# Optimization experiments

Measured on AMD Instinct MI355X. Metric: run time of the kernel, lower is better.

Reference implementation:

```python
import math
import jax, jax.numpy as jnp
import numpy as np
from jax.scipy.linalg import solve_triangular

K, D, Q = 512, 2048, 8
B = 8192
EPS = 1e-5
RHO0 = math.log(math.exp(1.0) - 1.0)  # softplus^-1(1.0), matches psi_init=scale_init=1.0


def setup_inputs() -> dict:
    key = jax.random.key(0)
    k1, k2, k3, k4, k5 = jax.random.split(key, 5)
    x = jax.random.normal(k1, (B, D), dtype=jnp.float32)
    mu = jax.random.normal(k2, (K, D), dtype=jnp.float32)          # centroids
    dir_raw = jax.random.normal(k3, (K, D, Q), dtype=jnp.float32) / math.sqrt(D)
    scale_rho = jnp.full((K, Q), RHO0, dtype=jnp.float32) + 0.01 * jax.random.normal(k4, (K, Q), dtype=jnp.float32)
    psi_rho = jnp.full((D,), RHO0, dtype=jnp.float32) + 0.01 * jax.random.normal(k5, (D,), dtype=jnp.float32)
    pi_logits = jnp.zeros((K,), dtype=jnp.float32)
    return {"x": x, "mu": mu, "dir_raw": dir_raw, "scale_rho": scale_rho,
            "psi_rho": psi_rho, "pi_logits": pi_logits}


def _nll(x, mu, dir_raw, scale_rho, psi_rho, pi_logits):
    Dd = x.shape[1]
    q = dir_raw.shape[2]
    # diagonal noise (shared across components since psi_per_component=False)
    psi = jax.nn.softplus(psi_rho) + EPS                      # (D,)
    psi_inv = 1.0 / psi                                       # (D,)
    # factor loadings W_k = normalize(dir_raw, dim=1) * softplus(scale)
    n = jnp.maximum(jnp.linalg.norm(dir_raw, axis=1, keepdims=True), EPS)
    W = (dir_raw / n) * jax.nn.softplus(scale_rho)[:, None, :]  # (K, D, q)
    # Woodbury inner matrix M_k = I + W^T Psi^{-1} W and its Cholesky
    A = W * jnp.sqrt(psi_inv)[None, :, None]                  # (K, D, q)
    M = jnp.einsum('kdi,kdj->kij', A, A) + jnp.eye(q, dtype=W.dtype)[None]
    L = jnp.linalg.cholesky(M)                                # (K, q, q) lower
    # quadratic form pieces
    xT_Pinv_x = (x ** 2) @ psi_inv                            # (B,)
    xT_Pinv_mu = x @ (psi_inv[None, :] * mu).T                # (B, K)
    muT_Pinv_mu = jnp.sum(mu ** 2 * psi_inv[None, :], axis=-1)  # (K,)
    quad_Psi = xT_Pinv_x[:, None] - 2.0 * xT_Pinv_mu + muT_Pinv_mu[None, :]
    PinvW = psi_inv[None, :, None] * W                        # (K, D, q)
    WT_Pinv_x = jnp.einsum('bd,kdq->bkq', x, PinvW)           # (B, K, q)
    WT_Pinv_mu = jnp.einsum('kd,kdq->kq', mu, PinvW)          # (K, q)
    v = WT_Pinv_x - WT_Pinv_mu[None, :, :]                    # (B, K, q)
    # Ez = M^{-1} v via the Cholesky factor (batched over K, rhs over B)
    vT = jnp.transpose(v, (1, 2, 0))                          # (K, q, B)
    y = solve_triangular(L, vT, lower=True)
    EzT = solve_triangular(jnp.swapaxes(L, -1, -2), y, lower=False)
    Ez = jnp.transpose(EzT, (2, 0, 1))                        # (B, K, q)
    quad = quad_Psi - jnp.sum(v * Ez, axis=-1)                # (B, K)
    # log-determinants via Woodbury: log|C| = log|Psi| + log|M|
    logdet_Psi = jnp.sum(jnp.log(psi))                        # scalar (shared psi)
    logdet_M = 2.0 * jnp.sum(jnp.log(jnp.diagonal(L, axis1=-2, axis2=-1)), axis=-1)  # (K,)
    logdet_C = logdet_Psi + logdet_M                          # (K,)
    ll = -0.5 * (Dd * math.log(2.0 * math.pi) + logdet_C[None, :] + quad)  # (B, K)
    log_pi = jax.nn.log_softmax(pi_logits)
    logp = jax.scipy.special.logsumexp(ll + log_pi[None, :], axis=1)  # (B,)
    return jnp.mean(-logp)


def reference(x, mu, dir_raw, scale_rho, psi_rho, pi_logits):
    return _nll(x, mu, dir_raw, scale_rho, psi_rho, pi_logits)
```

## Files before the change

kernel.cpp:

```cpp
#include <hip/hip_runtime.h>

constexpr int Bn = 8192;
constexpr int Dd = 2048;
constexpr int Kk = 512;
constexpr int Qq = 8;
constexpr int Nn = Kk * 9;
constexpr float DLOG2PI = 3763.9722f;

constexpr int BM = 256, BN = 144, BK = 128;

constexpr float SX = 16.f;
constexpr float SW = 64.f;
constexpr float SG = 16.f;
constexpr float INV_UW = 1.f / (16.f * 64.f);
constexpr float INV_UG = 1.f / (16.f * 16.f);

constexpr size_t OFF_PSI   = 0;
constexpr size_t OFF_LDP   = 8192;
constexpr size_t OFF_LOGPI = 8448;
constexpr size_t OFF_OFFK  = 10752;
constexpr size_t OFF_MINV  = 13056;
constexpr size_t OFF_XPX   = 144384;
constexpr size_t OFF_XBF   = 177408;
constexpr size_t OFF_GT    = 33731840;
constexpr size_t OFF_LL    = 52606208;
constexpr size_t OFF_PART  = 69383424;

typedef float f32x4 __attribute__((ext_vector_type(4)));
typedef int   i32x4v __attribute__((ext_vector_type(4)));
typedef int   i32x8v __attribute__((ext_vector_type(8)));

__device__ inline float softplusf(float x) {
  return fmaxf(x, 0.f) + log1pf(expf(-fabsf(x)));
}
__device__ inline unsigned short f2bf(float x) {
  unsigned int u = __builtin_bit_cast(unsigned int, x);
  u = (u + 0x7fffu + ((u >> 16) & 1u)) >> 16;
  return (unsigned short)u;
}
__device__ inline float bf2f(unsigned short u) {
  unsigned int v = ((unsigned int)u) << 16;
  return __builtin_bit_cast(float, v);
}
__device__ inline unsigned char f2fp8(float x) {
  int v = __builtin_amdgcn_cvt_pk_fp8_f32(x, 0.f, 0, false);
  return (unsigned char)(v & 0xff);
}
__device__ inline void glds16(const unsigned char* g, char* l) {
  __builtin_amdgcn_global_load_lds(
      (const __attribute__((address_space(1))) unsigned int*)g,
      (__attribute__((address_space(3))) unsigned int*)l, 16, 0, 0);
}
__device__ inline i32x8v ld_frag(const char* rowp, int quad, int s8) {
  i32x4v lo = *(const i32x4v*)(rowp + (((2 * quad)     ^ s8) * 16));
  i32x4v hi = *(const i32x4v*)(rowp + (((2 * quad + 1) ^ s8) * 16));
  i32x8v r;
  r[0] = lo[0]; r[1] = lo[1]; r[2] = lo[2]; r[3] = lo[3];
  r[4] = hi[0]; r[5] = hi[1]; r[6] = hi[2]; r[7] = hi[3];
  return r;
}

__global__ __launch_bounds__(256) void prep_psi(
    const float* __restrict__ psi_rho, const float* __restrict__ pi_logits,
    float* __restrict__ psi_inv, float* __restrict__ logdetPsi,
    float* __restrict__ logpi) {
  __shared__ float red[256];
  int t = threadIdx.x;
  float acc = 0.f;
  for (int d = t; d < Dd; d += 256) {
    float p = softplusf(psi_rho[d]) + 1e-5f;
    psi_inv[d] = 1.f / p;
    acc += logf(p);
  }
  red[t] = acc;
  __syncthreads();
  for (int s = 128; s > 0; s >>= 1) { if (t < s) red[t] += red[t + s]; __syncthreads(); }
  if (t == 0) *logdetPsi = red[0];
  __syncthreads();
  float mx = -3.4e38f;
  for (int i = t; i < Kk; i += 256) mx = fmaxf(mx, pi_logits[i]);
  red[t] = mx;
  __syncthreads();
  for (int s = 128; s > 0; s >>= 1) { if (t < s) red[t] = fmaxf(red[t], red[t + s]); __syncthreads(); }
  mx = red[0];
  __syncthreads();
  float se = 0.f;
  for (int i = t; i < Kk; i += 256) se += expf(pi_logits[i] - mx);
  red[t] = se;
  __syncthreads();
  for (int s = 128; s > 0; s >>= 1) { if (t < s) red[t] += red[t + s]; __syncthreads(); }
  float lse = mx + logf(red[0]);
  for (int i = t; i < Kk; i += 256) logpi[i] = pi_logits[i] - lse;
}

__global__ __launch_bounds__(256) void prep_k(
    const float* __restrict__ mu, const float* __restrict__ dir_raw,
    const float* __restrict__ scale_rho, const float* __restrict__ psi_inv,
    const float* __restrict__ logdetPsi, const float* __restrict__ logpi,
    float* __restrict__ offk, float* __restrict__ Minv,
    unsigned char* __restrict__ Gq) {
  __shared__ unsigned short sDir[Dd * 8];
  __shared__ float sPwmd[Dd];
  int k = blockIdx.x, t = threadIdx.x, lane = t & 63, w = t >> 6;
  float vals[53];
#pragma unroll
  for (int i = 0; i < 53; i++) vals[i] = 0.f;
  const float4* dirp = (const float4*)(dir_raw + (size_t)k * Dd * Qq);
  for (int d = t; d < Dd; d += 256) {
    float4 da = dirp[d * 2], db = dirp[d * 2 + 1];
    float dir8[8] = {da.x, da.y, da.z, da.w, db.x, db.y, db.z, db.w};
    float pw = psi_inv[d];
    float md = mu[(size_t)k * Dd + d];
    int c = 0;
#pragma unroll
    for (int i = 0; i < 8; i++) {
      float dip = dir8[i] * pw;
#pragma unroll
      for (int j = 0; j < 8; j++) {
        if (j < i) continue;
        vals[c] += dip * dir8[j]; c++;
      }
    }
#pragma unroll
    for (int q = 0; q < 8; q++) vals[36 + q] += dir8[q] * dir8[q];
    float mp = md * pw;
#pragma unroll
    for (int q = 0; q < 8; q++) vals[44 + q] += mp * dir8[q];
    vals[52] += md * mp;
#pragma unroll
    for (int q = 0; q < 8; q++) sDir[d * 8 + q] = f2bf(pw * dir8[q]);
    sPwmd[d] = mp;
  }
  __shared__ float redk[4 * 53];
#pragma unroll
  for (int v = 0; v < 53; v++) {
    float val = vals[v];
#pragma unroll
    for (int o = 32; o; o >>= 1) val += __shfl_down(val, o, 64);
    if (lane == 0) redk[w * 53 + v] = val;
  }
  __syncthreads();
  __shared__ float R[53];
  __shared__ float sAl[8], sAh[8];
  if (t < 53) R[t] = redk[t] + redk[53 + t] + redk[106 + t] + redk[159 + t];
  __syncthreads();
  if (t == 0) {
    float Sf[8][8];
    {
      int c2 = 0;
#pragma unroll
      for (int i = 0; i < 8; i++) {
#pragma unroll
        for (int j = 0; j < 8; j++) {
          if (j < i) continue;
          float v = R[c2++]; Sf[i][j] = v; Sf[j][i] = v;
        }
      }
    }
    float alpha[8];
#pragma unroll
    for (int q = 0; q < 8; q++) {
      float nr = fmaxf(sqrtf(R[36 + q]), 1e-5f);
      alpha[q] = softplusf(scale_rho[(size_t)k * 8 + q]) / nr;
    }
    float Mm[8][8];
#pragma unroll
    for (int i = 0; i < 8; i++)
#pragma unroll
      for (int j = 0; j < 8; j++)
        Mm[i][j] = alpha[i] * alpha[j] * Sf[i][j] + (i == j ? 1.f : 0.f);
    float L[8][8], Ld[8];
#pragma unroll
    for (int i = 0; i < 8; i++) {
#pragma unroll
      for (int j = 0; j < 8; j++) {
        if (j > i) continue;
        float s2 = Mm[i][j];
#pragma unroll
        for (int p = 0; p < 8; p++) { if (p < j) s2 -= L[i][p] * L[j][p]; }
        if (i == j) { L[i][i] = sqrtf(s2); Ld[i] = 1.f / L[i][i]; }
        else        L[i][j] = s2 * Ld[j];
      }
    }
    float logdetM = 0.f;
#pragma unroll
    for (int i = 0; i < 8; i++) logdetM += 2.f * logf(L[i][i]);
    float wv[8];
#pragma unroll
    for (int q = 0; q < 8; q++) wv[q] = alpha[q] * R[44 + q];
    float y[8], h[8];
#pragma unroll
    for (int i = 0; i < 8; i++) {
      float s2 = wv[i];
#pragma unroll
      for (int p = 0; p < 8; p++) { if (p < i) s2 -= L[i][p] * y[p]; }
      y[i] = s2 * Ld[i];
    }
#pragma unroll
    for (int i = 7; i >= 0; i--) {
      float s2 = y[i];
#pragma unroll
      for (int p = 0; p < 8; p++) { if (p > i) s2 -= L[p][i] * h[p]; }
      h[i] = s2 * Ld[i];
    }
    float cc = R[52];
#pragma unroll
    for (int q = 0; q < 8; q++) cc -= wv[q] * h[q];
#pragma unroll
    for (int col = 0; col < 8; col++) {
      float yy[8], z[8];
#pragma unroll
      for (int i = 0; i < 8; i++) {
        float s2 = (i == col) ? 1.f : 0.f;
#pragma unroll
        for (int p = 0; p < 8; p++) { if (p < i) s2 -= L[i][p] * yy[p]; }
        yy[i] = s2 * Ld[i];
      }
#pragma unroll
      for (int i = 7; i >= 0; i--) {
        float s2 = yy[i];
#pragma unroll
        for (int p = 0; p < 8; p++) { if (p > i) s2 -= L[p][i] * z[p]; }
        z[i] = s2 * Ld[i];
      }
#pragma unroll
      for (int r2 = 0; r2 < 8; r2++) Minv[(size_t)k * 64 + r2 * 8 + col] = z[r2];
    }
    offk[k] = -0.5f * (DLOG2PI + logdetPsi[0] + logdetM + cc) + logpi[k];
#pragma unroll
    for (int q = 0; q < 8; q++) { sAl[q] = alpha[q]; sAh[q] = alpha[q] * h[q]; }
  }
  __syncthreads();
  float al[8], ah[8];
#pragma unroll
  for (int q = 0; q < 8; q++) { al[q] = sAl[q]; ah[q] = sAh[q]; }
  for (int d = t; d < Dd; d += 256) {
    float pd[8];
#pragma unroll
    for (int q = 0; q < 8; q++) pd[q] = bf2f(sDir[d * 8 + q]);
    float gs = 0.f;
#pragma unroll
    for (int q = 0; q < 8; q++) {
      Gq[((size_t)(k * 9 + q)) * Dd + d] = f2fp8(SW * al[q] * pd[q]);
      gs += ah[q] * pd[q];
    }
    Gq[((size_t)(k * 9 + 8)) * Dd + d] = f2fp8(SG * (sPwmd[d] - gs));
  }
}

__global__ __launch_bounds__(256) void prep_x(
    const float* __restrict__ x, const float* __restrict__ psi_inv,
    unsigned char* __restrict__ xq, float* __restrict__ xPx) {
  int b = blockIdx.x, t = threadIdx.x, lane = t & 63, w = t >> 6;
  const float4* xr = (const float4*)(x + (size_t)b * Dd);
  const float4* pr = (const float4*)psi_inv;
  float4 v0 = xr[2 * t], v1 = xr[2 * t + 1];
  float4 p0 = pr[2 * t], p1 = pr[2 * t + 1];
  float acc = v0.x * v0.x * p0.x + v0.y * v0.y * p0.y + v0.z * v0.z * p0.z + v0.w * v0.w * p0.w
            + v1.x * v1.x * p1.x + v1.y * v1.y * p1.y + v1.z * v1.z * p1.z + v1.w * v1.w * p1.w;
  unsigned int q0 = (unsigned int)__builtin_amdgcn_cvt_pk_fp8_f32(SX * v0.x, SX * v0.y, 0, false);
  q0 = (unsigned int)__builtin_amdgcn_cvt_pk_fp8_f32(SX * v0.z, SX * v0.w, (int)q0, true);
  unsigned int q1 = (unsigned int)__builtin_amdgcn_cvt_pk_fp8_f32(SX * v1.x, SX * v1.y, 0, false);
  q1 = (unsigned int)__builtin_amdgcn_cvt_pk_fp8_f32(SX * v1.z, SX * v1.w, (int)q1, true);
  uint2 o; o.x = q0; o.y = q1;
  *(uint2*)(xq + (size_t)b * Dd + t * 8) = o;
#pragma unroll
  for (int s2 = 32; s2; s2 >>= 1) acc += __shfl_down(acc, s2, 64);
  __shared__ float r4[4];
  if (lane == 0) r4[w] = acc;
  __syncthreads();
  if (t == 0) xPx[b] = r4[0] + r4[1] + r4[2] + r4[3];
}

__global__ __launch_bounds__(256, 2) void gemm_ll(
    const unsigned char* __restrict__ xq, const unsigned char* __restrict__ Gq,
    const float* __restrict__ Minv, const float* __restrict__ offk,
    const float* __restrict__ xPx, float* __restrict__ ll) {
  __shared__ char smem[55424];
  float* Cs    = (float*)smem;
  float* sMinv = (float*)(smem + 51200);
  float* sOff  = (float*)(smem + 51200 + 4160);

  int t = threadIdx.x, lane = t & 63, w = t >> 6;
  int m0 = blockIdx.y * BM;
  int n0 = blockIdx.x * BN;
  int comp0 = blockIdx.x * 16;

  for (int i = t; i < 1024; i += 256) {
    int cl = i >> 6, idx = i & 63;
    sMinv[cl * 65 + idx] = Minv[(size_t)comp0 * 64 + i];
  }
  if (t < 16) sOff[t] = offk[comp0 + t];

  f32x4 acc[4][9];
  f32x4 zero = {0.f, 0.f, 0.f, 0.f};
#pragma unroll
  for (int mt = 0; mt < 4; mt++)
#pragma unroll
    for (int nt = 0; nt < 9; nt++) acc[mt][nt] = zero;

  int rr  = lane >> 3;
  int cph = lane & 7;
  int csw = cph ^ rr;
  int quad = lane >> 4, r16 = lane & 15;
  int s8 = r16 & 7;

#pragma unroll 1
  for (int k0 = 0; k0 < Dd; k0 += BK) {
    __syncthreads();
#pragma unroll
    for (int j = 0; j < 8; ++j) {
      int jj = w * 8 + j;
      glds16(xq + (size_t)(m0 + jj * 8 + rr) * Dd + k0 + csw * 16,
             smem + jj * 1024);
    }
    for (int jj = w; jj < 18; jj += 4) {
      glds16(Gq + (size_t)(n0 + jj * 8 + rr) * Dd + k0 + csw * 16,
             smem + 32768 + jj * 1024);
    }
    __syncthreads();
    i32x8v a0 = ld_frag(smem + (w * 64 +      r16) * 128, quad, s8);
    i32x8v a1 = ld_frag(smem + (w * 64 + 16 + r16) * 128, quad, s8);
    i32x8v a2 = ld_frag(smem + (w * 64 + 32 + r16) * 128, quad, s8);
    i32x8v a3 = ld_frag(smem + (w * 64 + 48 + r16) * 128, quad, s8);
#pragma unroll
    for (int nt = 0; nt < 9; ++nt) {
      i32x8v bv = ld_frag(smem + 32768 + (nt * 16 + r16) * 128, quad, s8);
      acc[0][nt] = __builtin_amdgcn_mfma_scale_f32_16x16x128_f8f6f4(
          a0, bv, acc[0][nt], 0, 0, 0, 0x7f7f7f7f, 0, 0x7f7f7f7f);
      acc[1][nt] = __builtin_amdgcn_mfma_scale_f32_16x16x128_f8f6f4(
          a1, bv, acc[1][nt], 0, 0, 0, 0x7f7f7f7f, 0, 0x7f7f7f7f);
      acc[2][nt] = __builtin_amdgcn_mfma_scale_f32_16x16x128_f8f6f4(
          a2, bv, acc[2][nt], 0, 0, 0, 0x7f7f7f7f, 0, 0x7f7f7f7f);
      acc[3][nt] = __builtin_amdgcn_mfma_scale_f32_16x16x128_f8f6f4(
          a3, bv, acc[3][nt], 0, 0, 0, 0x7f7f7f7f, 0, 0x7f7f7f7f);
    }
  }

  float P[36];
  {
    const float* Mi = sMinv + r16 * 65;
    int c = 0;
#pragma unroll
    for (int i2 = 0; i2 < 8; i2++) {
      P[c++] = 0.5f * Mi[i2 * 8 + i2];
#pragma unroll
      for (int j2 = i2 + 1; j2 < 8; j2++) P[c++] = Mi[i2 * 8 + j2];
    }
  }
  float offc = sOff[r16];

  __syncthreads();
  float* myC = Cs + w * (16 * 148);
#pragma unroll
  for (int mt = 0; mt < 4; ++mt) {
#pragma unroll
    for (int nt = 0; nt < 9; ++nt) {
#pragma unroll
      for (int r = 0; r < 4; r++) {
        myC[(quad * 4 + r) * 148 + nt * 16 + r16] = acc[mt][nt][r];
      }
    }
#pragma unroll
    for (int i = 0; i < 4; i++) {
      int row_l = quad + 4 * i;
      int b = m0 + w * 64 + mt * 16 + row_l;
      const float* cp = myC + row_l * 148 + r16 * 9;
      float u[8];
#pragma unroll
      for (int j = 0; j < 8; j++) u[j] = cp[j] * INV_UW;
      float s = cp[8] * INV_UG;
      float tq = 0.f;
      int c = 0;
#pragma unroll
      for (int i2 = 0; i2 < 8; i2++) {
        float s2 = P[c++] * u[i2];
#pragma unroll
        for (int j2 = i2 + 1; j2 < 8; j2++) s2 += P[c++] * u[j2];
        tq += u[i2] * s2;
      }
      ll[(size_t)b * Kk + comp0 + r16] = offc + s + tq - 0.5f * xPx[b];
    }
  }
}

__global__ __launch_bounds__(256) void lse_rows(
    const float* __restrict__ ll, float* __restrict__ part) {
  int t = threadIdx.x, lane = t & 63, w = t >> 6;
  int b = blockIdx.x * 4 + w;
  const float* row = ll + (size_t)b * Kk;
  float v[8];
  float mx = -3.4e38f;
#pragma unroll
  for (int i = 0; i < 8; i++) { v[i] = row[lane + 64 * i]; mx = fmaxf(mx, v[i]); }
#pragma unroll
  for (int o = 32; o; o >>= 1) mx = fmaxf(mx, __shfl_xor(mx, o, 64));
  float se = 0.f;
#pragma unroll
  for (int i = 0; i < 8; i++) se += expf(v[i] - mx);
#pragma unroll
  for (int o = 32; o; o >>= 1) se += __shfl_xor(se, o, 64);
  __shared__ float r4[4];
  if (lane == 0) r4[w] = -(mx + logf(se));
  __syncthreads();
  if (t == 0) part[blockIdx.x] = r4[0] + r4[1] + r4[2] + r4[3];
}

__global__ __launch_bounds__(256) void final_mean(
    const float* __restrict__ part, float* __restrict__ out) {
  int t = threadIdx.x, lane = t & 63, w = t >> 6;
  float acc = 0.f;
  for (int i = t; i < 2048; i += 256) acc += part[i];
#pragma unroll
  for (int o = 32; o; o >>= 1) acc += __shfl_down(acc, o, 64);
  __shared__ float r4[4];
  if (lane == 0) r4[w] = acc;
  __syncthreads();
  if (t == 0) out[0] = (r4[0] + r4[1] + r4[2] + r4[3]) * (1.0f / 8192.0f);
}

extern "C" void kernel_launch(void* const* d_in, const int* in_sizes, int n_in,
                              void* d_out, int out_size, void* d_ws, size_t ws_size,
                              hipStream_t stream) {
  const float* x         = (const float*)d_in[0];
  const float* mu        = (const float*)d_in[1];
  const float* dir_raw   = (const float*)d_in[2];
  const float* scale_rho = (const float*)d_in[3];
  const float* psi_rho   = (const float*)d_in[4];
  const float* pi_logits = (const float*)d_in[5];
  float* out = (float*)d_out;
  char* ws = (char*)d_ws;

  float* psi_inv          = (float*)(ws + OFF_PSI);
  float* logdetPsi        = (float*)(ws + OFF_LDP);
  float* logpi            = (float*)(ws + OFF_LOGPI);
  float* offk             = (float*)(ws + OFF_OFFK);
  float* Minv             = (float*)(ws + OFF_MINV);
  float* xPx              = (float*)(ws + OFF_XPX);
  unsigned char* xq       = (unsigned char*)(ws + OFF_XBF);
  unsigned char* Gq       = (unsigned char*)(ws + OFF_GT);
  float* ll               = (float*)(ws + OFF_LL);
  float* part             = (float*)(ws + OFF_PART);

  prep_psi<<<1, 256, 0, stream>>>(psi_rho, pi_logits, psi_inv, logdetPsi, logpi);
  prep_k<<<Kk, 256, 0, stream>>>(mu, dir_raw, scale_rho, psi_inv, logdetPsi, logpi,
                                 offk, Minv, Gq);
  prep_x<<<Bn, 256, 0, stream>>>(x, psi_inv, xq, xPx);
  dim3 g(Nn / BN, Bn / BM);
  gemm_ll<<<g, 256, 0, stream>>>(xq, Gq, Minv, offk, xPx, ll);
  lse_rows<<<Bn / 4, 256, 0, stream>>>(ll, part);
  final_mean<<<1, 256, 0, stream>>>(part, out);
}
```

Before: 241.0 us.

## Merge three prep kernels into one launch by recomputing psi_inv per block

Result: slower. 252.3 us (+4.7%).

```diff
diff --git a/kernel.cpp b/kernel.cpp
--- a/kernel.cpp
+++ b/kernel.cpp
@@ -15,7 +15,6 @@
 constexpr float INV_UW = 1.f / (16.f * 64.f);
 constexpr float INV_UG = 1.f / (16.f * 16.f);
 
-constexpr size_t OFF_PSI   = 0;
 constexpr size_t OFF_LDP   = 8192;
 constexpr size_t OFF_LOGPI = 8448;
 constexpr size_t OFF_OFFK  = 10752;
@@ -38,8 +37,11 @@
   u = (u + 0x7fffu + ((u >> 16) & 1u)) >> 16;
   return (unsigned short)u;
 }
-__device__ inline float bf2f(unsigned short u) {
-  unsigned int v = ((unsigned int)u) << 16;
+__device__ inline unsigned int pack2(float a, float b) {
+  return (unsigned int)f2bf(a) | ((unsigned int)f2bf(b) << 16);
+}
+__device__ inline float bf2f(unsigned int u16) {
+  unsigned int v = u16 << 16;
   return __builtin_bit_cast(float, v);
 }
 __device__ inline unsigned char f2fp8(float x) {
@@ -60,48 +62,79 @@
   return r;
 }
 
-__global__ __launch_bounds__(256) void prep_psi(
+__global__ __launch_bounds__(256) void prep_all(
+    const float* __restrict__ x, const float* __restrict__ mu,
+    const float* __restrict__ dir_raw, const float* __restrict__ scale_rho,
     const float* __restrict__ psi_rho, const float* __restrict__ pi_logits,
-    float* __restrict__ psi_inv, float* __restrict__ logdetPsi,
-    float* __restrict__ logpi) {
-  __shared__ float red[256];
-  int t = threadIdx.x;
-  float acc = 0.f;
-  for (int d = t; d < Dd; d += 256) {
-    float p = softplusf(psi_rho[d]) + 1e-5f;
-    psi_inv[d] = 1.f / p;
-    acc += logf(p);
-  }
-  red[t] = acc;
-  __syncthreads();
-  for (int s = 128; s > 0; s >>= 1) { if (t < s) red[t] += red[t + s]; __syncthreads(); }
-  if (t == 0) *logdetPsi = red[0];
-  __syncthreads();
-  float mx = -3.4e38f;
-  for (int i = t; i < Kk; i += 256) mx = fmaxf(mx, pi_logits[i]);
-  red[t] = mx;
-  __syncthreads();
-  for (int s = 128; s > 0; s >>= 1) { if (t < s) red[t] = fmaxf(red[t], red[t + s]); __syncthreads(); }
-  mx = red[0];
-  __syncthreads();
-  float se = 0.f;
-  for (int i = t; i < Kk; i += 256) se += expf(pi_logits[i] - mx);
-  red[t] = se;
-  __syncthreads();
-  for (int s = 128; s > 0; s >>= 1) { if (t < s) red[t] += red[t + s]; __syncthreads(); }
-  float lse = mx + logf(red[0]);
-  for (int i = t; i < Kk; i += 256) logpi[i] = pi_logits[i] - lse;
-}
-
-__global__ __launch_bounds__(256) void prep_k(
-    const float* __restrict__ mu, const float* __restrict__ dir_raw,
-    const float* __restrict__ scale_rho, const float* __restrict__ psi_inv,
-    const float* __restrict__ logdetPsi, const float* __restrict__ logpi,
+    float* __restrict__ logdetPsi, float* __restrict__ logpi,
     float* __restrict__ offk, float* __restrict__ Minv,
-    unsigned char* __restrict__ Gq) {
+    unsigned char* __restrict__ Gq, unsigned char* __restrict__ xq,
+    float* __restrict__ xPx) {
   __shared__ unsigned short sDir[Dd * 8];
   __shared__ float sPwmd[Dd];
-  int k = blockIdx.x, t = threadIdx.x, lane = t & 63, w = t >> 6;
+  __shared__ float redk[4 * 53];
+  __shared__ float R[53];
+  __shared__ float sAl[8], sAh[8];
+
+  int bid = blockIdx.x;
+  int t = threadIdx.x, lane = t & 63, w = t >> 6;
+
+  if (bid >= Kk + Bn) {
+    float* red = sPwmd;
+    float acc = 0.f;
+    for (int d = t; d < Dd; d += 256)
+      acc += logf(softplusf(psi_rho[d]) + 1e-5f);
+    red[t] = acc;
+    __syncthreads();
+    for (int s = 128; s > 0; s >>= 1) { if (t < s) red[t] += red[t + s]; __syncthreads(); }
+    if (t == 0) *logdetPsi = red[0];
+    __syncthreads();
+    float mx = -3.4e38f;
+    for (int i = t; i < Kk; i += 256) mx = fmaxf(mx, pi_logits[i]);
+    red[t] = mx;
+    __syncthreads();
+    for (int s = 128; s > 0; s >>= 1) { if (t < s) red[t] = fmaxf(red[t], red[t + s]); __syncthreads(); }
+    mx = red[0];
+    __syncthreads();
+    float se = 0.f;
+    for (int i = t; i < Kk; i += 256) se += expf(pi_logits[i] - mx);
+    red[t] = se;
+    __syncthreads();
+    for (int s = 128; s > 0; s >>= 1) { if (t < s) red[t] += red[t + s]; __syncthreads(); }
+    float lse = mx + logf(red[0]);
+    for (int i = t; i < Kk; i += 256) logpi[i] = pi_logits[i] - lse;
+    return;
+  }
+
+  if (bid >= Kk) {
+    int b = bid - Kk;
+    const float4* xr = (const float4*)(x + (size_t)b * Dd);
+    const float4* pr = (const float4*)psi_rho;
+    float4 v0 = xr[2 * t], v1 = xr[2 * t + 1];
+    float4 r0 = pr[2 * t], r1 = pr[2 * t + 1];
+    float4 p0, p1;
+    p0.x = 1.f / (softplusf(r0.x) + 1e-5f); p0.y = 1.f / (softplusf(r0.y) + 1e-5f);
+    p0.z = 1.f / (softplusf(r0.z) + 1e-5f); p0.w = 1.f / (softplusf(r0.w) + 1e-5f);
+    p1.x = 1.f / (softplusf(r1.x) + 1e-5f); p1.y = 1.f / (softplusf(r1.y) + 1e-5f);
+    p1.z = 1.f / (softplusf(r1.z) + 1e-5f); p1.w = 1.f / (softplusf(r1.w) + 1e-5f);
+    float acc = v0.x * v0.x * p0.x + v0.y * v0.y * p0.y + v0.z * v0.z * p0.z + v0.w * v0.w * p0.w
+              + v1.x * v1.x * p1.x + v1.y * v1.y * p1.y + v1.z * v1.z * p1.z + v1.w * v1.w * p1.w;
+    unsigned int q0 = (unsigned int)__builtin_amdgcn_cvt_pk_fp8_f32(SX * v0.x, SX * v0.y, 0, false);
+    q0 = (unsigned int)__builtin_amdgcn_cvt_pk_fp8_f32(SX * v0.z, SX * v0.w, (int)q0, true);
+    unsigned int q1 = (unsigned int)__builtin_amdgcn_cvt_pk_fp8_f32(SX * v1.x, SX * v1.y, 0, false);
+    q1 = (unsigned int)__builtin_amdgcn_cvt_pk_fp8_f32(SX * v1.z, SX * v1.w, (int)q1, true);
+    uint2 o; o.x = q0; o.y = q1;
+    *(uint2*)(xq + (size_t)b * Dd + t * 8) = o;
+#pragma unroll
+    for (int s2 = 32; s2; s2 >>= 1) acc += __shfl_down(acc, s2, 64);
+    float* r4 = sPwmd;
+    if (lane == 0) r4[w] = acc;
+    __syncthreads();
+    if (t == 0) xPx[b] = r4[0] + r4[1] + r4[2] + r4[3];
+    return;
+  }
+
+  int k = bid;
   float vals[53];
 #pragma unroll
   for (int i = 0; i < 53; i++) vals[i] = 0.f;
@@ -109,7 +142,7 @@
   for (int d = t; d < Dd; d += 256) {
     float4 da = dirp[d * 2], db = dirp[d * 2 + 1];
     float dir8[8] = {da.x, da.y, da.z, da.w, db.x, db.y, db.z, db.w};
-    float pw = psi_inv[d];
+    float pw = 1.f / (softplusf(psi_rho[d]) + 1e-5f);
     float md = mu[(size_t)k * Dd + d];
     int c = 0;
 #pragma unroll
@@ -127,11 +160,14 @@
 #pragma unroll
     for (int q = 0; q < 8; q++) vals[44 + q] += mp * dir8[q];
     vals[52] += md * mp;
-#pragma unroll
-    for (int q = 0; q < 8; q++) sDir[d * 8 + q] = f2bf(pw * dir8[q]);
+    uint4 pk;
+    pk.x = pack2(pw * dir8[0], pw * dir8[1]);
+    pk.y = pack2(pw * dir8[2], pw * dir8[3]);
+    pk.z = pack2(pw * dir8[4], pw * dir8[5]);
+    pk.w = pack2(pw * dir8[6], pw * dir8[7]);
+    *(uint4*)(sDir + d * 8) = pk;
     sPwmd[d] = mp;
   }
-  __shared__ float redk[4 * 53];
 #pragma unroll
   for (int v = 0; v < 53; v++) {
     float val = vals[v];
@@ -140,8 +176,6 @@
     if (lane == 0) redk[w * 53 + v] = val;
   }
   __syncthreads();
-  __shared__ float R[53];
-  __shared__ float sAl[8], sAh[8];
   if (t < 53) R[t] = redk[t] + redk[53 + t] + redk[106 + t] + redk[159 + t];
   __syncthreads();
   if (t == 0) {
@@ -226,7 +260,7 @@
 #pragma unroll
       for (int r2 = 0; r2 < 8; r2++) Minv[(size_t)k * 64 + r2 * 8 + col] = z[r2];
     }
-    offk[k] = -0.5f * (DLOG2PI + logdetPsi[0] + logdetM + cc) + logpi[k];
+    offk[k] = -0.5f * (DLOG2PI + logdetM + cc);
 #pragma unroll
     for (int q = 0; q < 8; q++) { sAl[q] = alpha[q]; sAh[q] = alpha[q] * h[q]; }
   }
@@ -235,9 +269,12 @@
 #pragma unroll
   for (int q = 0; q < 8; q++) { al[q] = sAl[q]; ah[q] = sAh[q]; }
   for (int d = t; d < Dd; d += 256) {
+    uint4 pk = *(const uint4*)(sDir + d * 8);
     float pd[8];
-#pragma unroll
-    for (int q = 0; q < 8; q++) pd[q] = bf2f(sDir[d * 8 + q]);
+    pd[0] = bf2f(pk.x & 0xffffu); pd[1] = bf2f(pk.x >> 16);
+    pd[2] = bf2f(pk.y & 0xffffu); pd[3] = bf2f(pk.y >> 16);
+    pd[4] = bf2f(pk.z & 0xffffu); pd[5] = bf2f(pk.z >> 16);
+    pd[6] = bf2f(pk.w & 0xffffu); pd[7] = bf2f(pk.w >> 16);
     float gs = 0.f;
 #pragma unroll
     for (int q = 0; q < 8; q++) {
@@ -248,33 +285,10 @@
   }
 }
 
-__global__ __launch_bounds__(256) void prep_x(
-    const float* __restrict__ x, const float* __restrict__ psi_inv,
-    unsigned char* __restrict__ xq, float* __restrict__ xPx) {
-  int b = blockIdx.x, t = threadIdx.x, lane = t & 63, w = t >> 6;
-  const float4* xr = (const float4*)(x + (size_t)b * Dd);
-  const float4* pr = (const float4*)psi_inv;
-  float4 v0 = xr[2 * t], v1 = xr[2 * t + 1];
-  float4 p0 = pr[2 * t], p1 = pr[2 * t + 1];
-  float acc = v0.x * v0.x * p0.x + v0.y * v0.y * p0.y + v0.z * v0.z * p0.z + v0.w * v0.w * p0.w
-            + v1.x * v1.x * p1.x + v1.y * v1.y * p1.y + v1.z * v1.z * p1.z + v1.w * v1.w * p1.w;
-  unsigned int q0 = (unsigned int)__builtin_amdgcn_cvt_pk_fp8_f32(SX * v0.x, SX * v0.y, 0, false);
-  q0 = (unsigned int)__builtin_amdgcn_cvt_pk_fp8_f32(SX * v0.z, SX * v0.w, (int)q0, true);
-  unsigned int q1 = (unsigned int)__builtin_amdgcn_cvt_pk_fp8_f32(SX * v1.x, SX * v1.y, 0, false);
-  q1 = (unsigned int)__builtin_amdgcn_cvt_pk_fp8_f32(SX * v1.z, SX * v1.w, (int)q1, true);
-  uint2 o; o.x = q0; o.y = q1;
-  *(uint2*)(xq + (size_t)b * Dd + t * 8) = o;
-#pragma unroll
-  for (int s2 = 32; s2; s2 >>= 1) acc += __shfl_down(acc, s2, 64);
-  __shared__ float r4[4];
-  if (lane == 0) r4[w] = acc;
-  __syncthreads();
-  if (t == 0) xPx[b] = r4[0] + r4[1] + r4[2] + r4[3];
-}
-
 __global__ __launch_bounds__(256, 2) void gemm_ll(
     const unsigned char* __restrict__ xq, const unsigned char* __restrict__ Gq,
     const float* __restrict__ Minv, const float* __restrict__ offk,
+    const float* __restrict__ logpi, const float* __restrict__ logdetPsi,
     const float* __restrict__ xPx, float* __restrict__ ll) {
   __shared__ char smem[55424];
   float* Cs    = (float*)smem;
@@ -290,7 +304,8 @@
     int cl = i >> 6, idx = i & 63;
     sMinv[cl * 65 + idx] = Minv[(size_t)comp0 * 64 + i];
   }
-  if (t < 16) sOff[t] = offk[comp0 + t];
+  if (t < 16)
+    sOff[t] = offk[comp0 + t] + logpi[comp0 + t] - 0.5f * logdetPsi[0];
 
   f32x4 acc[4][9];
   f32x4 zero = {0.f, 0.f, 0.f, 0.f};
@@ -431,7 +446,6 @@
   float* out = (float*)d_out;
   char* ws = (char*)d_ws;
 
-  float* psi_inv          = (float*)(ws + OFF_PSI);
   float* logdetPsi        = (float*)(ws + OFF_LDP);
   float* logpi            = (float*)(ws + OFF_LOGPI);
   float* offk             = (float*)(ws + OFF_OFFK);
@@ -442,12 +456,11 @@
   float* ll               = (float*)(ws + OFF_LL);
   float* part             = (float*)(ws + OFF_PART);
 
-  prep_psi<<<1, 256, 0, stream>>>(psi_rho, pi_logits, psi_inv, logdetPsi, logpi);
-  prep_k<<<Kk, 256, 0, stream>>>(mu, dir_raw, scale_rho, psi_inv, logdetPsi, logpi,
-                                 offk, Minv, Gq);
-  prep_x<<<Bn, 256, 0, stream>>>(x, psi_inv, xq, xPx);
+  prep_all<<<Kk + Bn + 1, 256, 0, stream>>>(x, mu, dir_raw, scale_rho, psi_rho,
+                                            pi_logits, logdetPsi, logpi, offk,
+                                            Minv, Gq, xq, xPx);
   dim3 g(Nn / BN, Bn / BM);
-  gemm_ll<<<g, 256, 0, stream>>>(xq, Gq, Minv, offk, xPx, ll);
+  gemm_ll<<<g, 256, 0, stream>>>(xq, Gq, Minv, offk, logpi, logdetPsi, xPx, ll);
   lse_rows<<<Bn / 4, 256, 0, stream>>>(ll, part);
   final_mean<<<1, 256, 0, stream>>>(part, out);
 }
```
